# Kernel tuning notes

Measured on AMD Instinct MI355X. Metric: run time of the kernel, lower is better.

Reference implementation:

```python
import jax, jax.numpy as jnp
import numpy as np

# static module config (matches init_kwargs)
DIM = 128
HEADS = 8
DW, HW, WW = 5, 7, 7  # depth/height/width window


def _neighbor_indices(D, H, W):
    """Flat circular-neighborhood indices, shape (P, n) with P=D*H*W, n=DW*HW*WW."""
    od = np.arange(DW) - (DW - 1) // 2
    oh = np.arange(HW) - (HW - 1) // 2
    ow = np.arange(WW) - (WW - 1) // 2
    dd = (np.arange(D)[:, None] + od[None, :]) % D   # (D, DW)
    hh = (np.arange(H)[:, None] + oh[None, :]) % H   # (H, HW)
    ww = (np.arange(W)[:, None] + ow[None, :]) % W   # (W, WW)
    idx = (dd[:, None, None, :, None, None] * (H * W)
           + hh[None, :, None, None, :, None] * W
           + ww[None, None, :, None, None, :])        # (D,H,W,DW,HW,WW)
    return jnp.asarray(idx.reshape(D * H * W, DW * HW * WW), dtype=jnp.int32)


def setup_inputs() -> dict:
    key = jax.random.key(0)
    k1, k2, k3, k4, k5 = jax.random.split(key, 5)
    B, D, H, W, C = 1, 5, 24, 48, DIM
    w_scale = 1.0 / np.sqrt(C)  # keep attention logits in a sane range
    return {
        "x": jax.random.normal(k1, (B, D, H, W, C), dtype=jnp.float32),
        "qkv_w": jax.random.normal(k2, (3 * C, C), dtype=jnp.float32) * w_scale,
        "qkv_b": jax.random.normal(k3, (3 * C,), dtype=jnp.float32) * 0.01,
        "proj_w": jax.random.normal(k4, (C, C), dtype=jnp.float32) * w_scale,
        "proj_b": jax.random.normal(k5, (C,), dtype=jnp.float32) * 0.01,
    }


def reference(x, qkv_w, qkv_b, proj_w, proj_b):
    B, D, H, W, C = x.shape
    P = D * H * W
    n = DW * HW * WW
    hd = C // HEADS
    scale = hd ** -0.5
    idx = _neighbor_indices(D, H, W)                      # (P, n) int32, static

    xf = x.reshape(B, P, C)
    qkv = xf @ qkv_w.T + qkv_b                            # (B, P, 3C)
    q, k, v = jnp.split(qkv, 3, axis=-1)

    q = q.reshape(B, P, HEADS, hd)                        # center-pixel query
    k_g = k[:, idx].reshape(B, P, n, HEADS, hd)           # gathered circular neighborhood
    v_g = v[:, idx].reshape(B, P, n, HEADS, hd)

    scores = jnp.einsum('bphd,bpnhd->bhpn', q, k_g) * scale
    attn = jax.nn.softmax(scores, axis=-1)                # softmax over 245 neighbors
    out = jnp.einsum('bhpn,bpnhd->bphd', attn, v_g).reshape(B, P, C)
    out = out @ proj_w.T + proj_b
    return out.reshape(B, D, H, W, C)
```

## Files before the change

### kernel.cpp

```cpp
#include <hip/hip_runtime.h>
#include <hip/hip_bf16.h>
#include <cstddef>

#define DIMC   128
#define NHEADS 8
#define HDIM   16
#define DD     5
#define HH     24
#define WW_    48
#define NPOS   (DD * HH * WW_)
#define SCALE  0.25f

typedef short    bf16x8 __attribute__((ext_vector_type(8)));
typedef float    f32x4  __attribute__((ext_vector_type(4)));
typedef unsigned u32x4  __attribute__((ext_vector_type(4)));

__device__ __forceinline__ unsigned short f2bf(float f) {
    unsigned u = __float_as_uint(f);
    u = (u + 0x7FFFu + ((u >> 16) & 1u)) >> 16;
    return (unsigned short)u;
}
__device__ __forceinline__ float bf2f(unsigned short s) {
    return __uint_as_float(((unsigned)s) << 16);
}
__device__ __forceinline__ unsigned cvt_pk_bf16(float a, float b) {
    unsigned r;
    asm("v_cvt_pk_bf16_f32 %0, %1, %2" : "=v"(r) : "v"(a), "v"(b));
    return r;
}
__device__ __forceinline__ float bfpk_lo(unsigned p) { return __uint_as_float(p << 16); }
__device__ __forceinline__ float bfpk_hi(unsigned p) { return __uint_as_float(p & 0xffff0000u); }
__device__ __forceinline__ bf16x8 pk4_to_bf16x8(unsigned a, unsigned b, unsigned c, unsigned d) {
    u32x4 t = {a, b, c, d};
    return __builtin_bit_cast(bf16x8, t);
}

__global__ __launch_bounds__(256, 3) void gemm_qkv_kernel(
    const float* __restrict__ x,
    const float* __restrict__ wq,
    const float* __restrict__ qkv_b,
    unsigned short* __restrict__ Qhl,
    unsigned short* __restrict__ Kbf,
    unsigned short* __restrict__ Vbf)
{
    __shared__ __align__(16) unsigned short Bs[64][264];

    const int tid = threadIdx.x;
    const int bn  = blockIdx.x * 64;
    const int bm  = blockIdx.y * 64;

    for (int i = tid; i < 2048; i += 256) {
        const int r = i >> 5, c4 = (i & 31) * 4;
        const float4 v = *(const float4*)(wq + (size_t)(bn + r) * 128 + c4);
        const unsigned h01 = cvt_pk_bf16(v.x, v.y);
        const unsigned h23 = cvt_pk_bf16(v.z, v.w);
        const unsigned l01 = cvt_pk_bf16(v.x - bfpk_lo(h01), v.y - bfpk_hi(h01));
        const unsigned l23 = cvt_pk_bf16(v.z - bfpk_lo(h23), v.w - bfpk_hi(h23));
        *(uint2*)(&Bs[r][c4])       = make_uint2(h01, h23);
        *(uint2*)(&Bs[r][128 + c4]) = make_uint2(l01, l23);
    }
    __syncthreads();

    const int w    = tid >> 6;
    const int lane = tid & 63;
    const int ln   = lane & 15;
    const int quad = lane >> 4;
    const int row  = bm + w * 16 + ln;
    const float* ar = x + (size_t)row * 128 + quad * 8;

    f32x4 acc[4] = {};
    #pragma unroll
    for (int kcg = 0; kcg < 4; ++kcg) {
        const float4 xa = *(const float4*)(ar + kcg * 32);
        const float4 xb = *(const float4*)(ar + kcg * 32 + 4);
        const unsigned h0 = cvt_pk_bf16(xa.x, xa.y);
        const unsigned h1 = cvt_pk_bf16(xa.z, xa.w);
        const unsigned h2 = cvt_pk_bf16(xb.x, xb.y);
        const unsigned h3 = cvt_pk_bf16(xb.z, xb.w);
        const unsigned l0 = cvt_pk_bf16(xa.x - bfpk_lo(h0), xa.y - bfpk_hi(h0));
        const unsigned l1 = cvt_pk_bf16(xa.z - bfpk_lo(h1), xa.w - bfpk_hi(h1));
        const unsigned l2 = cvt_pk_bf16(xb.x - bfpk_lo(h2), xb.y - bfpk_hi(h2));
        const unsigned l3 = cvt_pk_bf16(xb.z - bfpk_lo(h3), xb.w - bfpk_hi(h3));
        const bf16x8 ahi = pk4_to_bf16x8(h0, h1, h2, h3);
        const bf16x8 alo = pk4_to_bf16x8(l0, l1, l2, l3);
        #pragma unroll
        for (int nt = 0; nt < 4; ++nt) {
            const bf16x8 bhi = *(const bf16x8*)(&Bs[nt * 16 + ln][kcg * 32 + quad * 8]);
            const bf16x8 blo = *(const bf16x8*)(&Bs[nt * 16 + ln][128 + kcg * 32 + quad * 8]);
            acc[nt] = __builtin_amdgcn_mfma_f32_16x16x32_bf16(ahi, bhi, acc[nt], 0, 0, 0);
            acc[nt] = __builtin_amdgcn_mfma_f32_16x16x32_bf16(alo, bhi, acc[nt], 0, 0, 0);
            acc[nt] = __builtin_amdgcn_mfma_f32_16x16x32_bf16(ahi, blo, acc[nt], 0, 0, 0);
        }
    }

    #pragma unroll
    for (int nt = 0; nt < 4; ++nt) {
        const int col = bn + nt * 16 + ln;
        const float bv = qkv_b[col];
        #pragma unroll
        for (int r = 0; r < 4; ++r) {
            const int orow = bm + w * 16 + quad * 4 + r;
            const float val = acc[nt][r] + bv;
            if (col < 128) {
                const int h = col >> 4, ci = col & 15;
                const unsigned short hi = f2bf(val);
                Qhl[(size_t)orow * 256 + h * 32 + ci]      = hi;
                Qhl[(size_t)orow * 256 + h * 32 + 16 + ci] = f2bf(val - bf2f(hi));
            } else if (col < 256) {
                Kbf[(size_t)orow * 128 + (col - 128)] = f2bf(val);
            } else {
                Vbf[(size_t)orow * 128 + (col - 256)] = f2bf(val);
            }
        }
    }
}

__global__ __launch_bounds__(128, 2) void gemm_proj_kernel(
    const float* __restrict__ Opart,
    const float* __restrict__ Lpart,
    const float* __restrict__ wp,
    const float* __restrict__ proj_b,
    float* __restrict__ out)
{
    __shared__ __align__(16) unsigned short Bs[64][264];

    const int tid = threadIdx.x;
    const int bn  = blockIdx.x * 64;
    const int bm  = blockIdx.y * 32;

    for (int i = tid; i < 2048; i += 128) {
        const int r = i >> 5, c4 = (i & 31) * 4;
        const float4 v = *(const float4*)(wp + (size_t)(bn + r) * 128 + c4);
        const unsigned h01 = cvt_pk_bf16(v.x, v.y);
        const unsigned h23 = cvt_pk_bf16(v.z, v.w);
        const unsigned l01 = cvt_pk_bf16(v.x - bfpk_lo(h01), v.y - bfpk_hi(h01));
        const unsigned l23 = cvt_pk_bf16(v.z - bfpk_lo(h23), v.w - bfpk_hi(h23));
        *(uint2*)(&Bs[r][c4])       = make_uint2(h01, h23);
        *(uint2*)(&Bs[r][128 + c4]) = make_uint2(l01, l23);
    }
    __syncthreads();

    const int w    = tid >> 6;
    const int lane = tid & 63;
    const int ln   = lane & 15;
    const int quad = lane >> 4;
    const int row  = bm + w * 16 + ln;

    float linv[8];
    {
        const float4 l0a = *(const float4*)(Lpart + (size_t)row * 8);
        const float4 l0b = *(const float4*)(Lpart + (size_t)row * 8 + 4);
        const float4 l1a = *(const float4*)(Lpart + (size_t)(NPOS + row) * 8);
        const float4 l1b = *(const float4*)(Lpart + (size_t)(NPOS + row) * 8 + 4);
        linv[0] = 1.0f / (l0a.x + l1a.x); linv[1] = 1.0f / (l0a.y + l1a.y);
        linv[2] = 1.0f / (l0a.z + l1a.z); linv[3] = 1.0f / (l0a.w + l1a.w);
        linv[4] = 1.0f / (l0b.x + l1b.x); linv[5] = 1.0f / (l0b.y + l1b.y);
        linv[6] = 1.0f / (l0b.z + l1b.z); linv[7] = 1.0f / (l0b.w + l1b.w);
    }
    const float* o0 = Opart + (size_t)row * 128 + quad * 8;
    const float* o1 = o0 + (size_t)NPOS * 128;

    f32x4 acc[4] = {};
    #pragma unroll
    for (int kcg = 0; kcg < 4; ++kcg) {
        const float4 a0 = *(const float4*)(o0 + kcg * 32);
        const float4 a0b = *(const float4*)(o0 + kcg * 32 + 4);
        const float4 a1 = *(const float4*)(o1 + kcg * 32);
        const float4 a1b = *(const float4*)(o1 + kcg * 32 + 4);
        const float inv = linv[kcg * 2 + (quad >> 1)];
        const float v0 = (a0.x + a1.x) * inv,  v1 = (a0.y + a1.y) * inv;
        const float v2 = (a0.z + a1.z) * inv,  v3 = (a0.w + a1.w) * inv;
        const float v4 = (a0b.x + a1b.x) * inv, v5 = (a0b.y + a1b.y) * inv;
        const float v6 = (a0b.z + a1b.z) * inv, v7 = (a0b.w + a1b.w) * inv;
        const unsigned h0 = cvt_pk_bf16(v0, v1);
        const unsigned h1 = cvt_pk_bf16(v2, v3);
        const unsigned h2 = cvt_pk_bf16(v4, v5);
        const unsigned h3 = cvt_pk_bf16(v6, v7);
        const unsigned l0 = cvt_pk_bf16(v0 - bfpk_lo(h0), v1 - bfpk_hi(h0));
        const unsigned l1 = cvt_pk_bf16(v2 - bfpk_lo(h1), v3 - bfpk_hi(h1));
        const unsigned l2 = cvt_pk_bf16(v4 - bfpk_lo(h2), v5 - bfpk_hi(h2));
        const unsigned l3 = cvt_pk_bf16(v6 - bfpk_lo(h3), v7 - bfpk_hi(h3));
        const bf16x8 ahi = pk4_to_bf16x8(h0, h1, h2, h3);
        const bf16x8 alo = pk4_to_bf16x8(l0, l1, l2, l3);
        #pragma unroll
        for (int nt = 0; nt < 4; ++nt) {
            const bf16x8 bhi = *(const bf16x8*)(&Bs[nt * 16 + ln][kcg * 32 + quad * 8]);
            const bf16x8 blo = *(const bf16x8*)(&Bs[nt * 16 + ln][128 + kcg * 32 + quad * 8]);
            acc[nt] = __builtin_amdgcn_mfma_f32_16x16x32_bf16(ahi, bhi, acc[nt], 0, 0, 0);
            acc[nt] = __builtin_amdgcn_mfma_f32_16x16x32_bf16(alo, bhi, acc[nt], 0, 0, 0);
            acc[nt] = __builtin_amdgcn_mfma_f32_16x16x32_bf16(ahi, blo, acc[nt], 0, 0, 0);
        }
    }

    #pragma unroll
    for (int nt = 0; nt < 4; ++nt) {
        const int col = bn + nt * 16 + ln;
        const float bv = proj_b[col];
        #pragma unroll
        for (int r = 0; r < 4; ++r) {
            const int orow = bm + w * 16 + quad * 4 + r;
            out[(size_t)orow * 128 + col] = acc[nt][r] + bv;
        }
    }
}

__global__ __launch_bounds__(256, 4) void attn_kernel(
    const unsigned short* __restrict__ Qhl,
    const unsigned short* __restrict__ Kbf,
    const unsigned short* __restrict__ Vbf,
    float* __restrict__ Opart,
    float* __restrict__ Lpart)
{
    __shared__ __align__(16) char smem[26368];
    unsigned short (*Vt)[264] = (unsigned short(*)[264])smem;
    unsigned short (*Qb)[40]  = (unsigned short(*)[40])(smem + 8448);
    unsigned short* PwBase    = (unsigned short*)(smem + 14848);
    float* red_l              = (float*)(smem + 25088);
    float* redO               = (float*)smem;

    const int bx   = blockIdx.x;
    const int tile = bx >> 1;
    const int half = bx & 1;
    const int h    = blockIdx.y;
    const int ty0  = (tile / 12) * 4;
    const int tx0  = (tile % 12) * 4;
    const int tid  = threadIdx.x;

    for (int i = tid; i < 512; i += 256) {
        const int ul = i >> 1, hf8 = i & 1;
        const int u  = half * 256 + ul;
        if (u < 500) {
            const int dp = u / 100;
            const int rr = u - dp * 100;
            const int yy = rr / 10;
            const int xx = rr - yy * 10;
            int y = ty0 - 3 + yy; if (y < 0) y += HH;  if (y >= HH) y -= HH;
            int x = tx0 - 3 + xx; if (x < 0) x += WW_; if (x >= WW_) x -= WW_;
            const int g = (dp * HH + y) * WW_ + x;
            const bf16x8 v = *(const bf16x8*)(Vbf + (size_t)g * 128 + h * 16 + hf8 * 8);
            #pragma unroll
            for (int c = 0; c < 8; ++c) Vt[hf8 * 8 + c][ul] = (unsigned short)v[c];
        } else {
            #pragma unroll
            for (int c = 0; c < 8; ++c) Vt[hf8 * 8 + c][ul] = 0;
        }
    }
    for (int i = tid; i < 320; i += 256) {
        const int p = i >> 2, seg = i & 3;
        const int d = p >> 4, s = p & 15;
        const int sy = s >> 2, sx = s & 3;
        const int g = (d * HH + ty0 + sy) * WW_ + tx0 + sx;
        *(bf16x8*)(&Qb[p][seg * 8]) = *(const bf16x8*)(Qhl + (size_t)g * 256 + h * 32 + seg * 8);
    }
    __syncthreads();

    const int w    = tid >> 6;
    const int lane = tid & 63;
    const int ln   = lane & 15;
    const int quad = lane >> 4;
    const int sy   = ln >> 2, sx = ln & 3;

    unsigned short* Pw = PwBase + w * 1280;

    bf16x8 qf[5];
    #pragma unroll
    for (int mt = 0; mt < 5; ++mt)
        qf[mt] = *(const bf16x8*)(&Qb[mt * 16 + ln][quad * 8]);

    f32x4 Ow[5] = {};
    float lsum[5] = {};

    #pragma unroll
    for (int chunk = 0; chunk < 2; ++chunk) {
        const int u0g = (half * 8 + w * 2 + chunk) * 32;
        const int u0l = (w * 2 + chunk) * 32;

        int rowa, rowb;
        {
            const int ua = u0g + ln      < 500 ? u0g + ln      : 499;
            const int ub = u0g + 16 + ln < 500 ? u0g + 16 + ln : 499;
            int dp = ua / 100, rr = ua - dp * 100, yy = rr / 10, xx = rr - yy * 10;
            int y = ty0 - 3 + yy; if (y < 0) y += HH;  if (y >= HH) y -= HH;
            int x = tx0 - 3 + xx; if (x < 0) x += WW_; if (x >= WW_) x -= WW_;
            rowa = (dp * HH + y) * WW_ + x;
            dp = ub / 100; rr = ub - dp * 100; yy = rr / 10; xx = rr - yy * 10;
            y = ty0 - 3 + yy; if (y < 0) y += HH;  if (y >= HH) y -= HH;
            x = tx0 - 3 + xx; if (x < 0) x += WW_; if (x >= WW_) x -= WW_;
            rowb = (dp * HH + y) * WW_ + x;
        }
        const bf16x8 ka = *(const bf16x8*)(Kbf + (size_t)rowa * 128 + h * 16 + (quad & 1) * 8);
        const bf16x8 kb = *(const bf16x8*)(Kbf + (size_t)rowb * 128 + h * 16 + (quad & 1) * 8);

        bool msk[2][4];
        #pragma unroll
        for (int b = 0; b < 2; ++b)
            #pragma unroll
            for (int r = 0; r < 4; ++r) {
                const int u = u0g + 16 * b + 4 * quad + r;
                const int rr = u % 100;
                const int uy = rr / 10, ux = rr - uy * 10;
                msk[b][r] = (u < 500) && ((unsigned)(uy - sy) <= 6u)
                                      && ((unsigned)(ux - sx) <= 6u);
            }

        const bf16x8 vf = *(const bf16x8*)(&Vt[ln][u0l + quad * 8]);

        #pragma unroll
        for (int mt = 0; mt < 5; ++mt) {
            f32x4 s0 = __builtin_amdgcn_mfma_f32_16x16x32_bf16(
                ka, qf[mt], (f32x4){0.f, 0.f, 0.f, 0.f}, 0, 0, 0);
            f32x4 s1 = __builtin_amdgcn_mfma_f32_16x16x32_bf16(
                kb, qf[mt], (f32x4){0.f, 0.f, 0.f, 0.f}, 0, 0, 0);

            unsigned short* pw = Pw + (mt & 1) * 640 + ln * 40;
            #pragma unroll
            for (int b = 0; b < 2; ++b) {
                const f32x4 s = b ? s1 : s0;
                float ev[4];
                #pragma unroll
                for (int r = 0; r < 4; ++r)
                    ev[r] = msk[b][r] ? __expf(fmaf(s[r], SCALE, -8.0f)) : 0.f;
                const unsigned p01 = cvt_pk_bf16(ev[0], ev[1]);
                const unsigned p23 = cvt_pk_bf16(ev[2], ev[3]);
                lsum[mt] += bfpk_lo(p01) + bfpk_hi(p01) + bfpk_lo(p23) + bfpk_hi(p23);
                *(unsigned*)(pw + 16 * b + 4 * quad)     = p01;
                *(unsigned*)(pw + 16 * b + 4 * quad + 2) = p23;
            }
            const bf16x8 pf = *(const bf16x8*)(Pw + (mt & 1) * 640 + ln * 40 + quad * 8);
            Ow[mt] = __builtin_amdgcn_mfma_f32_16x16x32_bf16(vf, pf, Ow[mt], 0, 0, 0);
        }
    }

    #pragma unroll
    for (int mt = 0; mt < 5; ++mt) {
        lsum[mt] += __shfl_xor(lsum[mt], 16);
        lsum[mt] += __shfl_xor(lsum[mt], 32);
    }

    __syncthreads();

    if (quad == 0) {
        #pragma unroll
        for (int mt = 0; mt < 5; ++mt)
            red_l[w * 80 + mt * 16 + ln] = lsum[mt];
    }
    #pragma unroll
    for (int mt = 0; mt < 5; ++mt)
        #pragma unroll
        for (int r = 0; r < 4; ++r)
            redO[(size_t)((w * 5 + mt) * 16 + quad * 4 + r) * 16 + ln] = Ow[mt][r];
    __syncthreads();

    for (int i = tid; i < 1280; i += 256) {
        const int m = i >> 4, c = i & 15;
        const int mt = m >> 4, mloc = m & 15;
        float o = 0.f, l = 0.f;
        #pragma unroll
        for (int w4 = 0; w4 < 4; ++w4) {
            o += redO[(size_t)((w4 * 5 + mt) * 16 + c) * 16 + mloc];
            l += red_l[w4 * 80 + m];
        }
        const int qsy = (mloc >> 2), qsx = mloc & 3;
        const size_t g = (size_t)((mt * HH + ty0 + qsy) * WW_ + (tx0 + qsx));
        Opart[((size_t)half * NPOS + g) * 128 + h * HDIM + c] = o;
        if (c == 0) Lpart[((size_t)half * NPOS + g) * 8 + h] = l;
    }
}

extern "C" void kernel_launch(void* const* d_in, const int* in_sizes, int n_in,
                              void* d_out, int out_size, void* d_ws, size_t ws_size,
                              hipStream_t stream)
{
    const float* x      = (const float*)d_in[0];
    const float* qkv_w  = (const float*)d_in[1];
    const float* qkv_b  = (const float*)d_in[2];
    const float* proj_w = (const float*)d_in[3];
    const float* proj_b = (const float*)d_in[4];
    float* out = (float*)d_out;

    char* ws = (char*)d_ws;
    unsigned short* Qhl   = (unsigned short*)ws;  ws += (size_t)NPOS * 256 * 2;
    unsigned short* Kbf   = (unsigned short*)ws;  ws += (size_t)NPOS * 128 * 2;
    unsigned short* Vbf   = (unsigned short*)ws;  ws += (size_t)NPOS * 128 * 2;
    float*          Opart = (float*)ws;           ws += (size_t)2 * NPOS * 128 * 4;
    float*          Lpart = (float*)ws;           ws += (size_t)2 * NPOS * 8 * 4;

    {
        dim3 grid(384 / 64, NPOS / 64);
        gemm_qkv_kernel<<<grid, 256, 0, stream>>>(x, qkv_w, qkv_b, Qhl, Kbf, Vbf);
    }
    {
        dim3 grid(144, NHEADS);
        attn_kernel<<<grid, 256, 0, stream>>>(Qhl, Kbf, Vbf, Opart, Lpart);
    }
    {
        dim3 grid(DIMC / 64, NPOS / 32);
        gemm_proj_kernel<<<grid, 128, 0, stream>>>(Opart, Lpart, proj_w, proj_b, out);
    }
}
```

Baseline: 99.01 us.

## Drop split-key attention partials; normalize and emit bf16 hi/lo in attention

The attention kernel no longer splits each tile's 500 neighbor keys across two blocks. One block now covers all keys, normalizes by the softmax sum itself, and writes the result as a bf16 hi/lo pair ready for the projection GEMM. This removes the fp32 partial O/L buffers, their extra global traffic, and the combine-and-convert step in the projection kernel. The projection kernel also uses 64-row tiles with 256 threads. The cost is half as many attention blocks (576 instead of 1152) and more shared memory per block, which lowers parallelism in the attention stage.

Result: faster. 95.07 us (-4.0%).

```diff
diff --git a/kernel.cpp b/kernel.cpp
--- a/kernel.cpp
+++ b/kernel.cpp
@@ -115,9 +115,8 @@
     }
 }
 
-__global__ __launch_bounds__(128, 2) void gemm_proj_kernel(
-    const float* __restrict__ Opart,
-    const float* __restrict__ Lpart,
+__global__ __launch_bounds__(256, 3) void gemm_proj_kernel(
+    const unsigned short* __restrict__ Ahl,
     const float* __restrict__ wp,
     const float* __restrict__ proj_b,
     float* __restrict__ out)
@@ -126,9 +125,9 @@
 
     const int tid = threadIdx.x;
     const int bn  = blockIdx.x * 64;
-    const int bm  = blockIdx.y * 32;
-
-    for (int i = tid; i < 2048; i += 128) {
+    const int bm  = blockIdx.y * 64;
+
+    for (int i = tid; i < 2048; i += 256) {
         const int r = i >> 5, c4 = (i & 31) * 4;
         const float4 v = *(const float4*)(wp + (size_t)(bn + r) * 128 + c4);
         const unsigned h01 = cvt_pk_bf16(v.x, v.y);
@@ -145,43 +144,13 @@
     const int ln   = lane & 15;
     const int quad = lane >> 4;
     const int row  = bm + w * 16 + ln;
-
-    float linv[8];
-    {
-        const float4 l0a = *(const float4*)(Lpart + (size_t)row * 8);
-        const float4 l0b = *(const float4*)(Lpart + (size_t)row * 8 + 4);
-        const float4 l1a = *(const float4*)(Lpart + (size_t)(NPOS + row) * 8);
-        const float4 l1b = *(const float4*)(Lpart + (size_t)(NPOS + row) * 8 + 4);
-        linv[0] = 1.0f / (l0a.x + l1a.x); linv[1] = 1.0f / (l0a.y + l1a.y);
-        linv[2] = 1.0f / (l0a.z + l1a.z); linv[3] = 1.0f / (l0a.w + l1a.w);
-        linv[4] = 1.0f / (l0b.x + l1b.x); linv[5] = 1.0f / (l0b.y + l1b.y);
-        linv[6] = 1.0f / (l0b.z + l1b.z); linv[7] = 1.0f / (l0b.w + l1b.w);
-    }
-    const float* o0 = Opart + (size_t)row * 128 + quad * 8;
-    const float* o1 = o0 + (size_t)NPOS * 128;
+    const unsigned short* ar = Ahl + (size_t)row * 256 + (quad >> 1) * 32 + (quad & 1) * 8;
 
     f32x4 acc[4] = {};
     #pragma unroll
     for (int kcg = 0; kcg < 4; ++kcg) {
-        const float4 a0 = *(const float4*)(o0 + kcg * 32);
-        const float4 a0b = *(const float4*)(o0 + kcg * 32 + 4);
-        const float4 a1 = *(const float4*)(o1 + kcg * 32);
-        const float4 a1b = *(const float4*)(o1 + kcg * 32 + 4);
-        const float inv = linv[kcg * 2 + (quad >> 1)];
-        const float v0 = (a0.x + a1.x) * inv,  v1 = (a0.y + a1.y) * inv;
-        const float v2 = (a0.z + a1.z) * inv,  v3 = (a0.w + a1.w) * inv;
-        const float v4 = (a0b.x + a1b.x) * inv, v5 = (a0b.y + a1b.y) * inv;
-        const float v6 = (a0b.z + a1b.z) * inv, v7 = (a0b.w + a1b.w) * inv;
-        const unsigned h0 = cvt_pk_bf16(v0, v1);
-        const unsigned h1 = cvt_pk_bf16(v2, v3);
-        const unsigned h2 = cvt_pk_bf16(v4, v5);
-        const unsigned h3 = cvt_pk_bf16(v6, v7);
-        const unsigned l0 = cvt_pk_bf16(v0 - bfpk_lo(h0), v1 - bfpk_hi(h0));
-        const unsigned l1 = cvt_pk_bf16(v2 - bfpk_lo(h1), v3 - bfpk_hi(h1));
-        const unsigned l2 = cvt_pk_bf16(v4 - bfpk_lo(h2), v5 - bfpk_hi(h2));
-        const unsigned l3 = cvt_pk_bf16(v6 - bfpk_lo(h3), v7 - bfpk_hi(h3));
-        const bf16x8 ahi = pk4_to_bf16x8(h0, h1, h2, h3);
-        const bf16x8 alo = pk4_to_bf16x8(l0, l1, l2, l3);
+        const bf16x8 ahi = *(const bf16x8*)(ar + kcg * 64);
+        const bf16x8 alo = *(const bf16x8*)(ar + kcg * 64 + 16);
         #pragma unroll
         for (int nt = 0; nt < 4; ++nt) {
             const bf16x8 bhi = *(const bf16x8*)(&Bs[nt * 16 + ln][kcg * 32 + quad * 8]);
@@ -208,30 +177,26 @@
     const unsigned short* __restrict__ Qhl,
     const unsigned short* __restrict__ Kbf,
     const unsigned short* __restrict__ Vbf,
-    float* __restrict__ Opart,
-    float* __restrict__ Lpart)
+    unsigned short* __restrict__ Ahl)
 {
-    __shared__ __align__(16) char smem[26368];
-    unsigned short (*Vt)[264] = (unsigned short(*)[264])smem;
-    unsigned short (*Qb)[40]  = (unsigned short(*)[40])(smem + 8448);
-    unsigned short* PwBase    = (unsigned short*)(smem + 14848);
-    float* red_l              = (float*)(smem + 25088);
+    __shared__ __align__(16) char smem[34560];
+    unsigned short (*Vt)[520] = (unsigned short(*)[520])smem;
+    unsigned short (*Qb)[40]  = (unsigned short(*)[40])(smem + 16640);
+    unsigned short* PwBase    = (unsigned short*)(smem + 23040);
+    float* red_l              = (float*)(smem + 33280);
     float* redO               = (float*)smem;
 
-    const int bx   = blockIdx.x;
-    const int tile = bx >> 1;
-    const int half = bx & 1;
+    const int tile = blockIdx.x;
     const int h    = blockIdx.y;
     const int ty0  = (tile / 12) * 4;
     const int tx0  = (tile % 12) * 4;
     const int tid  = threadIdx.x;
 
-    for (int i = tid; i < 512; i += 256) {
+    for (int i = tid; i < 1024; i += 256) {
         const int ul = i >> 1, hf8 = i & 1;
-        const int u  = half * 256 + ul;
-        if (u < 500) {
-            const int dp = u / 100;
-            const int rr = u - dp * 100;
+        if (ul < 500) {
+            const int dp = ul / 100;
+            const int rr = ul - dp * 100;
             const int yy = rr / 10;
             const int xx = rr - yy * 10;
             int y = ty0 - 3 + yy; if (y < 0) y += HH;  if (y >= HH) y -= HH;
@@ -271,14 +236,13 @@
     float lsum[5] = {};
 
     #pragma unroll
-    for (int chunk = 0; chunk < 2; ++chunk) {
-        const int u0g = (half * 8 + w * 2 + chunk) * 32;
-        const int u0l = (w * 2 + chunk) * 32;
+    for (int chunk = 0; chunk < 4; ++chunk) {
+        const int u0 = (w * 4 + chunk) * 32;
 
         int rowa, rowb;
         {
-            const int ua = u0g + ln      < 500 ? u0g + ln      : 499;
-            const int ub = u0g + 16 + ln < 500 ? u0g + 16 + ln : 499;
+            const int ua = u0 + ln      < 500 ? u0 + ln      : 499;
+            const int ub = u0 + 16 + ln < 500 ? u0 + 16 + ln : 499;
             int dp = ua / 100, rr = ua - dp * 100, yy = rr / 10, xx = rr - yy * 10;
             int y = ty0 - 3 + yy; if (y < 0) y += HH;  if (y >= HH) y -= HH;
             int x = tx0 - 3 + xx; if (x < 0) x += WW_; if (x >= WW_) x -= WW_;
@@ -296,14 +260,14 @@
         for (int b = 0; b < 2; ++b)
             #pragma unroll
             for (int r = 0; r < 4; ++r) {
-                const int u = u0g + 16 * b + 4 * quad + r;
+                const int u = u0 + 16 * b + 4 * quad + r;
                 const int rr = u % 100;
                 const int uy = rr / 10, ux = rr - uy * 10;
                 msk[b][r] = (u < 500) && ((unsigned)(uy - sy) <= 6u)
                                       && ((unsigned)(ux - sx) <= 6u);
             }
 
-        const bf16x8 vf = *(const bf16x8*)(&Vt[ln][u0l + quad * 8]);
+        const bf16x8 vf = *(const bf16x8*)(&Vt[ln][u0 + quad * 8]);
 
         #pragma unroll
         for (int mt = 0; mt < 5; ++mt) {
@@ -360,10 +324,12 @@
             o += redO[(size_t)((w4 * 5 + mt) * 16 + c) * 16 + mloc];
             l += red_l[w4 * 80 + m];
         }
+        const float val = o / l;
         const int qsy = (mloc >> 2), qsx = mloc & 3;
         const size_t g = (size_t)((mt * HH + ty0 + qsy) * WW_ + (tx0 + qsx));
-        Opart[((size_t)half * NPOS + g) * 128 + h * HDIM + c] = o;
-        if (c == 0) Lpart[((size_t)half * NPOS + g) * 8 + h] = l;
+        const unsigned short hi = f2bf(val);
+        Ahl[g * 256 + h * 32 + c]      = hi;
+        Ahl[g * 256 + h * 32 + 16 + c] = f2bf(val - bf2f(hi));
     }
 }
 
@@ -379,22 +345,21 @@
     float* out = (float*)d_out;
 
     char* ws = (char*)d_ws;
-    unsigned short* Qhl   = (unsigned short*)ws;  ws += (size_t)NPOS * 256 * 2;
-    unsigned short* Kbf   = (unsigned short*)ws;  ws += (size_t)NPOS * 128 * 2;
-    unsigned short* Vbf   = (unsigned short*)ws;  ws += (size_t)NPOS * 128 * 2;
-    float*          Opart = (float*)ws;           ws += (size_t)2 * NPOS * 128 * 4;
-    float*          Lpart = (float*)ws;           ws += (size_t)2 * NPOS * 8 * 4;
+    unsigned short* Qhl = (unsigned short*)ws;  ws += (size_t)NPOS * 256 * 2;
+    unsigned short* Kbf = (unsigned short*)ws;  ws += (size_t)NPOS * 128 * 2;
+    unsigned short* Vbf = (unsigned short*)ws;  ws += (size_t)NPOS * 128 * 2;
+    unsigned short* Ahl = (unsigned short*)ws;  ws += (size_t)NPOS * 256 * 2;
 
     {
         dim3 grid(384 / 64, NPOS / 64);
         gemm_qkv_kernel<<<grid, 256, 0, stream>>>(x, qkv_w, qkv_b, Qhl, Kbf, Vbf);
     }
     {
-        dim3 grid(144, NHEADS);
-        attn_kernel<<<grid, 256, 0, stream>>>(Qhl, Kbf, Vbf, Opart, Lpart);
+        dim3 grid(72, NHEADS);
+        attn_kernel<<<grid, 256, 0, stream>>>(Qhl, Kbf, Vbf, Ahl);
     }
     {
-        dim3 grid(DIMC / 64, NPOS / 32);
-        gemm_proj_kernel<<<grid, 128, 0, stream>>>(Opart, Lpart, proj_w, proj_b, out);
-    }
-}
+        dim3 grid(DIMC / 64, NPOS / 64);
+        gemm_proj_kernel<<<grid, 256, 0, stream>>>(Ahl, proj_w, proj_b, out);
+    }
+}
```
